# Kernel optimization log

Hardware: AMD Instinct MI355X
Metric: run time of the kernel (lower is better)

## Reference

```python
import jax, jax.numpy as jnp
import numpy as np
from jax import lax

B, C, H, W, K, R = 8, 64, 128, 128, 3, 4  # batch, channels, height, width, kernel_size, region_number


def _leaky(x):
    return jnp.where(x >= 0, x, 0.1 * x)


def _asign_index(kernel, guide):
    # kernel: (b,R,c,h,w), guide: (b,R,h,w) -> hard top-1 region routing -> (b,c,h,w)
    mask = jax.nn.one_hot(jnp.argmax(guide, axis=1), R, axis=1, dtype=kernel.dtype)  # (b,R,h,w)
    return jnp.sum(kernel * mask[:, :, None], axis=1)


def _conv2d(x, w, pad):
    return lax.conv_general_dilated(x, w, (1, 1), [(pad, pad), (pad, pad)],
                                    dimension_numbers=('NCHW', 'OIHW', 'NCHW'))


def setup_inputs() -> dict:
    key = jax.random.key(0)
    ks = jax.random.split(key, 12)
    s = 0.05
    return {
        'x0': jax.random.normal(ks[0], (B, C, H, W), jnp.float32),
        'deg': jax.random.normal(ks[1], (B, C), jnp.float32),
        'q_map': jax.random.normal(ks[2], (B, 1, H, W), jnp.float32),
        'w_k1': jax.random.normal(ks[3], (C, C), jnp.float32) * s,
        'w_k2': jax.random.normal(ks[4], (R, C * K * K, C // R), jnp.float32) * s,
        'w_conv': jax.random.normal(ks[5], (C, C), jnp.float32) * s,
        'b_conv': jax.random.normal(ks[6], (C,), jnp.float32) * s,
        'w_ca1': jax.random.normal(ks[7], (C, C), jnp.float32) * s,
        'w_ca2': jax.random.normal(ks[8], (R, C, C // R), jnp.float32) * s,
        'w_g1': jax.random.normal(ks[9], (R, 1, K, K), jnp.float32) * s,
        'b_g1': jnp.zeros((R,), jnp.float32),
        'w_g2': jax.random.normal(ks[10], (R, 1, K, K), jnp.float32) * s,
        'b_g2': jnp.zeros((R,), jnp.float32),
    }


def reference(x0, deg, q_map, w_k1, w_k2, w_conv, b_conv, w_ca1, w_ca2, w_g1, b_g1, w_g2, b_g2):
    b, c, h, w = x0.shape
    pad = (K - 1) // 2
    # --- dynamic per-sample, per-channel depthwise kernels from degradation rep ---
    y = _leaky(deg @ w_k1.T)                                             # 1x1 conv1d -> (b, c)
    kflat = jnp.einsum('bgi,goi->bgo', y.reshape(b, R, c // R), w_k2)    # grouped 1x1 conv1d
    kernel = kflat.reshape(b, R, c, K, K).transpose(0, 2, 1, 3, 4)       # (b,c,R,K,K)
    rhs = kernel.reshape(b * c * R, 1, K, K)
    out = lax.conv_general_dilated(x0.reshape(1, b * c, h, w), rhs, (1, 1),
                                   [(pad, pad), (pad, pad)],
                                   dimension_numbers=('NCHW', 'OIHW', 'NCHW'),
                                   feature_group_count=b * c)            # (1, b*c*R, h, w)
    out = _leaky(out).reshape(b, c, R, h, w).transpose(0, 2, 1, 3, 4)    # (b,R,c,h,w)
    g1 = _conv2d(q_map, w_g1, 1) + b_g1[None, :, None, None]             # (b,R,h,w)
    out = _asign_index(out, g1)                                          # (b,c,h,w)
    out = jnp.einsum('bchw,oc->bohw', out, w_conv) + b_conv[None, :, None, None]
    # --- channel-attention (CA_layer) branch ---
    a = _leaky(deg @ w_ca1.T)                                            # (b, c)
    att = jax.nn.sigmoid(jnp.einsum('bgi,goi->bgo', a.reshape(b, R, c // R), w_ca2))  # (b,R,c)
    out2 = x0[:, None] * att[:, :, :, None, None]                        # (b,R,c,h,w)
    g2 = _conv2d(q_map, w_g2, 1) + b_g2[None, :, None, None]
    out2 = _asign_index(out2, g2)
    return out + out2
```

## Files before the change

kernel.cpp:

```cpp
#include <hip/hip_runtime.h>
#include <hip/hip_bf16.h>
#include <math.h>

#define Bn 8
#define Cn 64
#define Hn 128
#define Wn 128
#define Rn 4

typedef __bf16 v8bf __attribute__((ext_vector_type(8)));
typedef float  v16f __attribute__((ext_vector_type(16)));

__device__ __forceinline__ float leaky(float x) { return x >= 0.f ? x : 0.1f * x; }

__device__ __forceinline__ unsigned bf16pair(float a, float b) {
    __hip_bfloat16 ha = __float2bfloat16(a);
    __hip_bfloat16 hb = __float2bfloat16(b);
    return (unsigned)*reinterpret_cast<unsigned short*>(&ha) |
           ((unsigned)*reinterpret_cast<unsigned short*>(&hb) << 16);
}

__device__ __forceinline__ float dpp_up1(float x) {
    int r = __builtin_amdgcn_update_dpp(0, __builtin_bit_cast(int, x),
                                        0x138 , 0xf, 0xf, true);
    return __builtin_bit_cast(float, r);
}
__device__ __forceinline__ float dpp_down1(float x) {
    int r = __builtin_amdgcn_update_dpp(0, __builtin_bit_cast(int, x),
                                        0x130 , 0xf, 0xf, true);
    return __builtin_bit_cast(float, r);
}

__global__ __launch_bounds__(256) void precomp_kernel(
    const float* __restrict__ deg, const float* __restrict__ w_k1,
    const float* __restrict__ w_k2, const float* __restrict__ w_ca1,
    const float* __restrict__ w_ca2, const float* __restrict__ w_conv,
    float* __restrict__ kern_g, float* __restrict__ att_g,
    unsigned short* __restrict__ wbf)
{
    const int tid = threadIdx.x;
    if (blockIdx.x == Bn) {
        for (int f = tid; f < Cn * Cn; f += 256) {
            __hip_bfloat16 hx = __float2bfloat16(w_conv[f]);
            wbf[f] = *reinterpret_cast<unsigned short*>(&hx);
        }
        return;
    }
    const int b = blockIdx.x;
    __shared__ float y_s[64], a_s[64];
    if (tid < 64) {
        float sy = 0.f, sa = 0.f;
#pragma unroll 8
        for (int j = 0; j < 64; ++j) {
            float d = deg[b * 64 + j];
            sy += d * w_k1[tid * 64 + j];
            sa += d * w_ca1[tid * 64 + j];
        }
        y_s[tid] = leaky(sy);
        a_s[tid] = leaky(sa);
    }
    __syncthreads();
    for (int f = tid; f < Cn * Rn * 9; f += 256) {
        int c = f / 36;
        int j = f - c * 36;
        int r = j / 9;
        int kk = j - r * 9;
        int o = c * 9 + kk;
        const float* wp = &w_k2[(r * 576 + o) * 16];
        const float* yp = &y_s[r * 16];
        float s = 0.f;
#pragma unroll
        for (int i = 0; i < 16; ++i) s += yp[i] * wp[i];
        kern_g[b * 3072 + c * 48 + r * 12 + kk] = s;
    }
    {
        int r = tid >> 6, o = tid & 63;
        const float* wp = &w_ca2[(r * 64 + o) * 16];
        const float* ap = &a_s[r * 16];
        float s = 0.f;
#pragma unroll
        for (int i = 0; i < 16; ++i) s += ap[i] * wp[i];
        att_g[b * 256 + tid] = 1.f / (1.f + expf(-s));
    }
}

__global__ __launch_bounds__(512) void da_main(
    const float* __restrict__ x0, const float* __restrict__ q_map,
    const unsigned short* __restrict__ wbf, const float* __restrict__ b_conv,
    const float* __restrict__ w_g1, const float* __restrict__ b_g1,
    const float* __restrict__ w_g2, const float* __restrict__ b_g2,
    const float* __restrict__ kern_g, const float* __restrict__ att_g,
    float* __restrict__ out)
{
    __shared__ __align__(16) float kern_lds[Cn * 48];
    __shared__ __align__(16) unsigned short wc_lds[8][Cn][8];
    __shared__ __align__(16) unsigned short t_lds[Wn * Cn];
    __shared__ float att_lds[Rn * 68];
    __shared__ float bias_lds[Cn];
    __shared__ unsigned ridx[Wn];

    const int tid = threadIdx.x;
    const int ob = blockIdx.x;
    const int sb = ((ob & 7) << 7) | (ob >> 3);
    const int b = sb >> 7;
    const int h = sb & 127;

    const int lane = tid & 63;
    const int g = tid >> 6;
    const int w0 = 2 * lane;
    const int w1 = w0 + 1;

    for (int f = tid; f < Cn * 48; f += 512)
        kern_lds[f] = kern_g[b * 3072 + f];
    {
        int cq = tid & 7, o = tid >> 3;
        *(v8bf*)&wc_lds[cq][o][0] = *(const v8bf*)&wbf[o * 64 + cq * 8];
    }
    if (tid < 256) att_lds[(tid >> 6) * 68 + (tid & 63)] = att_g[b * 256 + tid];
    if (tid < 64) bias_lds[tid] = b_conv[tid];

    if (tid < 128) {
        const int wc = tid;
        float qv[9];
#pragma unroll
        for (int dh = 0; dh < 3; ++dh) {
            int row = h - 1 + dh;
#pragma unroll
            for (int dw = 0; dw < 3; ++dw) {
                int col = wc - 1 + dw;
                qv[dh * 3 + dw] = (row >= 0 && row < Hn && col >= 0 && col < Wn)
                                      ? q_map[(b * Hn + row) * Wn + col] : 0.f;
            }
        }
        float best1 = -1e30f, best2 = -1e30f;
        int r1 = 0, r2 = 0;
#pragma unroll
        for (int r = 0; r < Rn; ++r) {
            float s1 = b_g1[r], s2 = b_g2[r];
#pragma unroll
            for (int k = 0; k < 9; ++k) {
                s1 += qv[k] * w_g1[r * 9 + k];
                s2 += qv[k] * w_g2[r * 9 + k];
            }
            if (s1 > best1) { best1 = s1; r1 = r; }
            if (s2 > best2) { best2 = s2; r2 = r; }
        }
        ridx[wc] = (unsigned)r1 | ((unsigned)r2 << 16);
    }
    __syncthreads();

    const bool okm = (h > 0);
    const bool okp = (h < Hn - 1);
    const float* xbase = x0 + (size_t)(b * Cn) * Hn * Wn + h * Wn + w0;
    const int r1a = (int)(ridx[w0] & 0xffffu);
    const int r1b = (int)(ridx[w1] & 0xffffu);
    const int swz = (lane & 7) << 4;

    float2 b0m, b00, b0p;
    float2 b1m, b10, b1p;

#define LOADC(CI, BM, B0, BP)                                             \
    do {                                                                  \
        const float* xc = xbase + (8 * g + (CI)) * (Hn * Wn);             \
        BM = okm ? *(const float2*)(xc - Wn) : make_float2(0.f, 0.f);     \
        B0 = *(const float2*)xc;                                          \
        BP = okp ? *(const float2*)(xc + Wn) : make_float2(0.f, 0.f);     \
    } while (0)

    float tp0 = 0.f, tp1 = 0.f;
    LOADC(0, b0m, b00, b0p);
    LOADC(1, b1m, b10, b1p);
#pragma unroll
    for (int ci = 0; ci < 8; ++ci) {
        float2 avm, av0, avp;
        if ((ci & 1) == 0) { avm = b0m; av0 = b00; avp = b0p; }
        else               { avm = b1m; av0 = b10; avp = b1p; }
        if (ci < 6) {
            if ((ci & 1) == 0) LOADC(ci + 2, b0m, b00, b0p);
            else               LOADC(ci + 2, b1m, b10, b1p);
        }

        float lm = dpp_up1(avm.y),  l0 = dpp_up1(av0.y),  lp = dpp_up1(avp.y);
        float rm = dpp_down1(avm.x), r0 = dpp_down1(av0.x), rp = dpp_down1(avp.x);

        const int c = 8 * g + ci;
        const float* kpa = &kern_lds[c * 48 + r1a * 12];
        float4 a03 = *(const float4*)kpa;
        float4 a47 = *(const float4*)(kpa + 4);
        float a8 = kpa[8];
        float t0 = lm    * a03.x + avm.x * a03.y + avm.y * a03.z
                 + l0    * a03.w + av0.x * a47.x + av0.y * a47.y
                 + lp    * a47.z + avp.x * a47.w + avp.y * a8;
        const float* kpb = &kern_lds[c * 48 + r1b * 12];
        float4 b03 = *(const float4*)kpb;
        float4 b47 = *(const float4*)(kpb + 4);
        float b8 = kpb[8];
        float t1 = avm.x * b03.x + avm.y * b03.y + rm    * b03.z
                 + av0.x * b03.w + av0.y * b47.x + r0    * b47.y
                 + avp.x * b47.z + avp.y * b47.w + rp    * b8;
        t0 = leaky(t0);
        t1 = leaky(t1);

        if (ci & 1) {
            unsigned q0 = bf16pair(tp0, t0);
            unsigned q1 = bf16pair(tp1, t1);
            const int cbyte = (8 * g + ci - 1) * 2;
            *(unsigned*)((char*)t_lds + w0 * 128 + (cbyte ^ swz)) = q0;
            *(unsigned*)((char*)t_lds + w1 * 128 + (cbyte ^ swz)) = q1;
        } else {
            tp0 = t0;
            tp1 = t1;
        }
    }
#undef LOADC
    __syncthreads();

    const int v = tid >> 6;
    const int wt = v & 3;
    const int oh = v >> 2;
    const int col = lane & 31;
    const int kh = lane >> 5;
    const int wn = wt * 32 + col;

    v8bf Bf[4];
#pragma unroll
    for (int ks = 0; ks < 4; ++ks) {
        int cbyte = (16 * ks + 8 * kh) * 2;
        Bf[ks] = *(const v8bf*)((const char*)t_lds + wn * 128 +
                                (cbyte ^ (((wn >> 1) & 7) << 4)));
    }

    v16f acc;
#pragma unroll
    for (int i = 0; i < 16; ++i) acc[i] = 0.f;

#pragma unroll
    for (int ks = 0; ks < 4; ++ks) {
        const int cq = 2 * ks + kh;
        v8bf Af = *(const v8bf*)&wc_lds[cq][oh * 32 + col][0];
        acc = __builtin_amdgcn_mfma_f32_32x32x16_bf16(Af, Bf[ks], acc, 0, 0, 0);
    }

    const int r2e = (int)(ridx[wn] >> 16);
    const float* xcol = x0 + ((size_t)(b * Cn + oh * 32) * Hn + h) * Wn + wn;
    float* ocol = out + ((size_t)(b * Cn + oh * 32) * Hn + h) * Wn + wn;

#pragma unroll
    for (int r = 0; r < 16; ++r) {
        int row = (r & 3) + 8 * (r >> 2) + 4 * kh;
        int o = oh * 32 + row;
        float xv = xcol[(size_t)row * (Hn * Wn)];
        float res = acc[r] + bias_lds[o] + xv * att_lds[r2e * 68 + o];
        ocol[(size_t)row * (Hn * Wn)] = res;
    }
}

extern "C" void kernel_launch(void* const* d_in, const int* in_sizes, int n_in,
                              void* d_out, int out_size, void* d_ws, size_t ws_size,
                              hipStream_t stream)
{
    const float* x0     = (const float*)d_in[0];
    const float* deg    = (const float*)d_in[1];
    const float* q_map  = (const float*)d_in[2];
    const float* w_k1   = (const float*)d_in[3];
    const float* w_k2   = (const float*)d_in[4];
    const float* w_conv = (const float*)d_in[5];
    const float* b_conv = (const float*)d_in[6];
    const float* w_ca1  = (const float*)d_in[7];
    const float* w_ca2  = (const float*)d_in[8];
    const float* w_g1   = (const float*)d_in[9];
    const float* b_g1   = (const float*)d_in[10];
    const float* w_g2   = (const float*)d_in[11];
    const float* b_g2   = (const float*)d_in[12];
    float* outp   = (float*)d_out;
    float* kern_g = (float*)d_ws;
    float* att_g  = kern_g + Bn * 3072;
    unsigned short* wbf = (unsigned short*)(att_g + Bn * 256);

    precomp_kernel<<<Bn + 1, 256, 0, stream>>>(deg, w_k1, w_k2, w_ca1, w_ca2,
                                               w_conv, kern_g, att_g, wbf);
    da_main<<<Bn * Hn, 512, 0, stream>>>(x0, q_map, wbf, b_conv,
                                         w_g1, b_g1, w_g2, b_g2,
                                         kern_g, att_g, outp);
}
```

Baseline: 33.62 us.

## Process two output rows per block to reuse halo loads and setup

Each block now handles two adjacent image rows with 1024 threads instead of one row with 512 threads. Each thread loads four input rows, covering both output rows' 3x3 stencil, instead of three rows per output row, and the per-block staging of kernels, weights and attention into LDS is amortized over twice the work. The cost is a doubled t_lds buffer, halving the grid to 512 blocks, and larger blocks that may reduce occupancy or scheduling flexibility.

```diff
diff --git a/kernel.cpp b/kernel.cpp
--- a/kernel.cpp
+++ b/kernel.cpp
@@ -84,7 +84,7 @@
     }
 }
 
-__global__ __launch_bounds__(512) void da_main(
+__global__ __launch_bounds__(1024) void da_main(
     const float* __restrict__ x0, const float* __restrict__ q_map,
     const unsigned short* __restrict__ wbf, const float* __restrict__ b_conv,
     const float* __restrict__ w_g1, const float* __restrict__ b_g1,
@@ -94,37 +94,40 @@
 {
     __shared__ __align__(16) float kern_lds[Cn * 48];
     __shared__ __align__(16) unsigned short wc_lds[8][Cn][8];
-    __shared__ __align__(16) unsigned short t_lds[Wn * Cn];
+    __shared__ __align__(16) unsigned short t_lds[2][Wn * Cn];
     __shared__ float att_lds[Rn * 68];
     __shared__ float bias_lds[Cn];
-    __shared__ unsigned ridx[Wn];
+    __shared__ unsigned ridx[2][Wn];
 
     const int tid = threadIdx.x;
     const int ob = blockIdx.x;
-    const int sb = ((ob & 7) << 7) | (ob >> 3);
-    const int b = sb >> 7;
-    const int h = sb & 127;
+    const int sb = ((ob & 7) << 6) | (ob >> 3);
+    const int b = sb >> 6;
+    const int hp = sb & 63;
+    const int h0 = 2 * hp;
 
     const int lane = tid & 63;
     const int g = tid >> 6;
     const int w0 = 2 * lane;
     const int w1 = w0 + 1;
 
-    for (int f = tid; f < Cn * 48; f += 512)
+    for (int f = tid; f < Cn * 48; f += 1024)
         kern_lds[f] = kern_g[b * 3072 + f];
-    {
+    if (tid < 512) {
         int cq = tid & 7, o = tid >> 3;
         *(v8bf*)&wc_lds[cq][o][0] = *(const v8bf*)&wbf[o * 64 + cq * 8];
     }
     if (tid < 256) att_lds[(tid >> 6) * 68 + (tid & 63)] = att_g[b * 256 + tid];
     if (tid < 64) bias_lds[tid] = b_conv[tid];
 
-    if (tid < 128) {
-        const int wc = tid;
+    if (tid < 256) {
+        const int rr = tid >> 7;
+        const int wc = tid & 127;
+        const int row0 = h0 + rr;
         float qv[9];
 #pragma unroll
         for (int dh = 0; dh < 3; ++dh) {
-            int row = h - 1 + dh;
+            int row = row0 - 1 + dh;
 #pragma unroll
             for (int dw = 0; dw < 3; ++dw) {
                 int col = wc - 1 + dw;
@@ -145,88 +148,102 @@
             if (s1 > best1) { best1 = s1; r1 = r; }
             if (s2 > best2) { best2 = s2; r2 = r; }
         }
-        ridx[wc] = (unsigned)r1 | ((unsigned)r2 << 16);
+        ridx[rr][wc] = (unsigned)r1 | ((unsigned)r2 << 16);
     }
     __syncthreads();
 
-    const bool okm = (h > 0);
-    const bool okp = (h < Hn - 1);
-    const float* xbase = x0 + (size_t)(b * Cn) * Hn * Wn + h * Wn + w0;
-    const int r1a = (int)(ridx[w0] & 0xffffu);
-    const int r1b = (int)(ridx[w1] & 0xffffu);
+    const bool okm = (h0 > 0);
+    const bool okp = (hp < 63);
+    const float* xbase = x0 + ((size_t)(b * Cn) * Hn + h0) * Wn + w0;
+    const int r1a0 = (int)(ridx[0][w0] & 0xffffu);
+    const int r1b0 = (int)(ridx[0][w1] & 0xffffu);
+    const int r1a1 = (int)(ridx[1][w0] & 0xffffu);
+    const int r1b1 = (int)(ridx[1][w1] & 0xffffu);
     const int swz = (lane & 7) << 4;
 
-    float2 b0m, b00, b0p;
-    float2 b1m, b10, b1p;
-
-#define LOADC(CI, BM, B0, BP)                                             \
+    float2 nA, nB, nC, nD;
+
+#define LOADC(CI)                                                         \
     do {                                                                  \
-        const float* xc = xbase + (8 * g + (CI)) * (Hn * Wn);             \
-        BM = okm ? *(const float2*)(xc - Wn) : make_float2(0.f, 0.f);     \
-        B0 = *(const float2*)xc;                                          \
-        BP = okp ? *(const float2*)(xc + Wn) : make_float2(0.f, 0.f);     \
+        const float* xc = xbase + (4 * g + (CI)) * (Hn * Wn);             \
+        nA = okm ? *(const float2*)(xc - Wn) : make_float2(0.f, 0.f);     \
+        nB = *(const float2*)xc;                                          \
+        nC = *(const float2*)(xc + Wn);                                   \
+        nD = okp ? *(const float2*)(xc + 2 * Wn) : make_float2(0.f, 0.f); \
     } while (0)
 
-    float tp0 = 0.f, tp1 = 0.f;
-    LOADC(0, b0m, b00, b0p);
-    LOADC(1, b1m, b10, b1p);
-#pragma unroll
-    for (int ci = 0; ci < 8; ++ci) {
-        float2 avm, av0, avp;
-        if ((ci & 1) == 0) { avm = b0m; av0 = b00; avp = b0p; }
-        else               { avm = b1m; av0 = b10; avp = b1p; }
-        if (ci < 6) {
-            if ((ci & 1) == 0) LOADC(ci + 2, b0m, b00, b0p);
-            else               LOADC(ci + 2, b1m, b10, b1p);
-        }
-
-        float lm = dpp_up1(avm.y),  l0 = dpp_up1(av0.y),  lp = dpp_up1(avp.y);
-        float rm = dpp_down1(avm.x), r0 = dpp_down1(av0.x), rp = dpp_down1(avp.x);
-
-        const int c = 8 * g + ci;
-        const float* kpa = &kern_lds[c * 48 + r1a * 12];
+    float tp00 = 0.f, tp01 = 0.f, tp10 = 0.f, tp11 = 0.f;
+    LOADC(0);
+#pragma unroll
+    for (int ci = 0; ci < 4; ++ci) {
+        float2 A = nA, B = nB, C = nC, D = nD;
+        if (ci < 3) LOADC(ci + 1);
+
+        float lA = dpp_up1(A.y), lB = dpp_up1(B.y), lC = dpp_up1(C.y), lD = dpp_up1(D.y);
+        float rA = dpp_down1(A.x), rB = dpp_down1(B.x), rC = dpp_down1(C.x), rD = dpp_down1(D.x);
+
+        const int c = 4 * g + ci;
+        const float* kc = &kern_lds[c * 48];
+        const float* kpa = kc + r1a0 * 12;
         float4 a03 = *(const float4*)kpa;
         float4 a47 = *(const float4*)(kpa + 4);
         float a8 = kpa[8];
-        float t0 = lm    * a03.x + avm.x * a03.y + avm.y * a03.z
-                 + l0    * a03.w + av0.x * a47.x + av0.y * a47.y
-                 + lp    * a47.z + avp.x * a47.w + avp.y * a8;
-        const float* kpb = &kern_lds[c * 48 + r1b * 12];
+        float t00 = lA  * a03.x + A.x * a03.y + A.y * a03.z
+                  + lB  * a03.w + B.x * a47.x + B.y * a47.y
+                  + lC  * a47.z + C.x * a47.w + C.y * a8;
+        const float* kpb = kc + r1b0 * 12;
         float4 b03 = *(const float4*)kpb;
         float4 b47 = *(const float4*)(kpb + 4);
         float b8 = kpb[8];
-        float t1 = avm.x * b03.x + avm.y * b03.y + rm    * b03.z
-                 + av0.x * b03.w + av0.y * b47.x + r0    * b47.y
-                 + avp.x * b47.z + avp.y * b47.w + rp    * b8;
-        t0 = leaky(t0);
-        t1 = leaky(t1);
+        float t01 = A.x * b03.x + A.y * b03.y + rA  * b03.z
+                  + B.x * b03.w + B.y * b47.x + rB  * b47.y
+                  + C.x * b47.z + C.y * b47.w + rC  * b8;
+        const float* kpc = kc + r1a1 * 12;
+        float4 c03 = *(const float4*)kpc;
+        float4 c47 = *(const float4*)(kpc + 4);
+        float c8 = kpc[8];
+        float t10 = lB  * c03.x + B.x * c03.y + B.y * c03.z
+                  + lC  * c03.w + C.x * c47.x + C.y * c47.y
+                  + lD  * c47.z + D.x * c47.w + D.y * c8;
+        const float* kpd = kc + r1b1 * 12;
+        float4 d03 = *(const float4*)kpd;
+        float4 d47 = *(const float4*)(kpd + 4);
+        float d8 = kpd[8];
+        float t11 = B.x * d03.x + B.y * d03.y + rB  * d03.z
+                  + C.x * d03.w + C.y * d47.x + rC  * d47.y
+                  + D.x * d47.z + D.y * d47.w + rD  * d8;
+
+        t00 = leaky(t00); t01 = leaky(t01);
+        t10 = leaky(t10); t11 = leaky(t11);
 
         if (ci & 1) {
-            unsigned q0 = bf16pair(tp0, t0);
-            unsigned q1 = bf16pair(tp1, t1);
-            const int cbyte = (8 * g + ci - 1) * 2;
-            *(unsigned*)((char*)t_lds + w0 * 128 + (cbyte ^ swz)) = q0;
-            *(unsigned*)((char*)t_lds + w1 * 128 + (cbyte ^ swz)) = q1;
+            const int cbyte = (4 * g + ci - 1) * 2;
+            *(unsigned*)((char*)&t_lds[0][0] + w0 * 128 + (cbyte ^ swz)) = bf16pair(tp00, t00);
+            *(unsigned*)((char*)&t_lds[0][0] + w1 * 128 + (cbyte ^ swz)) = bf16pair(tp01, t01);
+            *(unsigned*)((char*)&t_lds[1][0] + w0 * 128 + (cbyte ^ swz)) = bf16pair(tp10, t10);
+            *(unsigned*)((char*)&t_lds[1][0] + w1 * 128 + (cbyte ^ swz)) = bf16pair(tp11, t11);
         } else {
-            tp0 = t0;
-            tp1 = t1;
+            tp00 = t00; tp01 = t01; tp10 = t10; tp11 = t11;
         }
     }
 #undef LOADC
     __syncthreads();
 
     const int v = tid >> 6;
-    const int wt = v & 3;
-    const int oh = v >> 2;
+    const int rr = v >> 3;
+    const int u = v & 7;
+    const int wt = u & 3;
+    const int oh = u >> 2;
     const int col = lane & 31;
     const int kh = lane >> 5;
     const int wn = wt * 32 + col;
+    const int h = h0 + rr;
 
     v8bf Bf[4];
 #pragma unroll
     for (int ks = 0; ks < 4; ++ks) {
         int cbyte = (16 * ks + 8 * kh) * 2;
-        Bf[ks] = *(const v8bf*)((const char*)t_lds + wn * 128 +
+        Bf[ks] = *(const v8bf*)((const char*)&t_lds[rr][0] + wn * 128 +
                                 (cbyte ^ (((wn >> 1) & 7) << 4)));
     }
 
@@ -241,7 +258,7 @@
         acc = __builtin_amdgcn_mfma_f32_32x32x16_bf16(Af, Bf[ks], acc, 0, 0, 0);
     }
 
-    const int r2e = (int)(ridx[wn] >> 16);
+    const int r2e = (int)(ridx[rr][wn] >> 16);
     const float* xcol = x0 + ((size_t)(b * Cn + oh * 32) * Hn + h) * Wn + wn;
     float* ocol = out + ((size_t)(b * Cn + oh * 32) * Hn + h) * Wn + wn;
 
@@ -279,7 +296,7 @@
 
     precomp_kernel<<<Bn + 1, 256, 0, stream>>>(deg, w_k1, w_k2, w_ca1, w_ca2,
                                                w_conv, kern_g, att_g, wbf);
-    da_main<<<Bn * Hn, 512, 0, stream>>>(x0, q_map, wbf, b_conv,
-                                         w_g1, b_g1, w_g2, b_g2,
-                                         kern_g, att_g, outp);
-}
+    da_main<<<Bn * (Hn / 2), 1024, 0, stream>>>(x0, q_map, wbf, b_conv,
+                                                w_g1, b_g1, w_g2, b_g2,
+                                                kern_g, att_g, outp);
+}
```

Result: slower. 35.41 us (+5.3%).
